# Kernel optimization log

Measured on AMD Instinct MI355X. Metric: run time of the kernel, lower is better.

Reference implementation:

```python
import jax, jax.numpy as jnp
import numpy as np

EMBED_DIM = 768
NUM_HEADS = 12
HEAD_DIM = EMBED_DIM // NUM_HEADS
SCALING = HEAD_DIM ** (-0.5)


def setup_inputs() -> dict:
    key = jax.random.key(0)
    ks = jax.random.split(key, 10)
    R, C, B, E = 128, 256, 1, EMBED_DIM
    x = jax.random.normal(ks[0], (R, C, B, E), dtype=jnp.float32)
    pad_mask = jax.random.randint(ks[1], (B, C), 0, 2).astype(bool)
    s = 1.0 / np.sqrt(E)
    wq = jax.random.normal(ks[2], (E, E), dtype=jnp.float32) * s
    bq = jnp.zeros((E,), dtype=jnp.float32)
    wk = jax.random.normal(ks[3], (E, E), dtype=jnp.float32) * s
    bk = jnp.zeros((E,), dtype=jnp.float32)
    wv = jax.random.normal(ks[4], (E, E), dtype=jnp.float32) * s
    bv = jnp.zeros((E,), dtype=jnp.float32)
    wo = jax.random.normal(ks[5], (E, E), dtype=jnp.float32) * s
    bo = jnp.zeros((E,), dtype=jnp.float32)
    return {"x": x, "self_attn_padding_mask": pad_mask,
            "wq": wq, "bq": bq, "wk": wk, "bk": bk,
            "wv": wv, "bv": bv, "wo": wo, "bo": bo}


def reference(x, self_attn_padding_mask, wq, bq, wk, bk, wv, bv, wo, bo):
    # x: [num_rows R, num_cols C, batch B, embed E]
    R, C, B, E = x.shape
    H, D = NUM_HEADS, HEAD_DIM
    q = (x @ wq.T + bq).reshape(R, C, B, H, D) * SCALING
    k = (x @ wk.T + bk).reshape(R, C, B, H, D)
    v = (x @ wv.T + bv).reshape(R, C, B, H, D)
    # attention over rows, independent per column c and batch n
    attn_weights = jnp.einsum('icnhd,jcnhd->hcnij', q, k)  # [H,C,B,R,R]
    if self_attn_padding_mask is not None:
        # mask: [B,C] -> mask all keys j for padded columns (same for all j)
        m = self_attn_padding_mask.T[None, :, :, None, None]  # [1,C,B,1,1]
        attn_weights = jnp.where(m, jnp.float32(-10000.0), attn_weights)
    attn_probs = jax.nn.softmax(attn_weights, axis=-1)
    context = jnp.einsum('hcnij,jcnhd->icnhd', attn_probs, v)
    context = context.reshape(R, C, B, E)
    output = context @ wo.T + bo
    return output, attn_probs
```

## Files before the change

### kernel.cpp

```cpp
#include <hip/hip_runtime.h>


typedef __attribute__((ext_vector_type(8))) __bf16 bf16x8;
typedef __attribute__((ext_vector_type(4))) float f32x4;
typedef unsigned short u16;
typedef unsigned int u32;

constexpr size_t TE = (size_t)32768 * 768;
constexpr int VSTRIDE = 256 * 1536;

__device__ __forceinline__ u16 f2b(float f) {
    u32 u = __builtin_bit_cast(u32, f);
    u += 0x7FFFu + ((u >> 16) & 1u);
    return (u16)(u >> 16);
}
__device__ __forceinline__ void split2(float f, u16& h, u16& l) {
    u32 u = __builtin_bit_cast(u32, f);
    h = (u16)(u >> 16);
    float rest = f - __builtin_bit_cast(float, u & 0xFFFF0000u);
    l = (u16)(__builtin_bit_cast(u32, rest) >> 16);
}

union B8 { bf16x8 v; u16 s[8]; uint4 q; };

__global__ __launch_bounds__(256) void convert_w3(
    const float* __restrict__ Wq, const float* __restrict__ Wk,
    const float* __restrict__ Wv, u16* __restrict__ slots)
{
    const int m = blockIdx.y;
    const float* src = (m == 0) ? Wq : ((m == 1) ? Wk : Wv);
    const int idx = blockIdx.x * 256 + threadIdx.x;
    const int r = idx / 96, k0 = (idx % 96) * 8;
    float4 f0 = *(const float4*)(src + (size_t)r * 768 + k0);
    float4 f1 = *(const float4*)(src + (size_t)r * 768 + k0 + 4);
    B8 h, l;
    split2(f0.x, h.s[0], l.s[0]); split2(f0.y, h.s[1], l.s[1]);
    split2(f0.z, h.s[2], l.s[2]); split2(f0.w, h.s[3], l.s[3]);
    split2(f1.x, h.s[4], l.s[4]); split2(f1.y, h.s[5], l.s[5]);
    split2(f1.z, h.s[6], l.s[6]); split2(f1.w, h.s[7], l.s[7]);
    *(uint4*)&slots[(size_t)1536 * (m * 1536 + r) + k0] = h.q;
    *(uint4*)&slots[(size_t)1536 * (m * 1536 + 768 + r) + k0] = l.q;
}

template <int MODE>
__global__ __launch_bounds__(256) void gemm_proj(
    const float* __restrict__ A, const u16* __restrict__ wsl, int wbase,
    const float* __restrict__ bias, u16* __restrict__ dst, float scale)
{
    const int wg = ((blockIdx.x & 7) * 192) + (blockIdx.x >> 3);
    const int tm = wg / 6, tn = wg - tm * 6;
    const int tid = threadIdx.x;
    const int lane = tid & 63, w = tid >> 6;
    const int l16 = lane & 15, quad = lane >> 4;
    const int wr = w >> 1, wc = w & 1;

    __shared__ u16 Ah[2][128][4][8], Al[2][128][4][8];

    f32x4 acc[4][4];
#pragma unroll
    for (int a = 0; a < 4; ++a)
#pragma unroll
        for (int b = 0; b < 4; ++b) acc[a][b] = (f32x4){0.f, 0.f, 0.f, 0.f};

    const int row0 = tid >> 3, kq = tid & 7;
    const int c8 = kq >> 1, o4 = (kq & 1) * 4;
    const float* ap = A + ((size_t)tm * 128 + row0) * 768 + kq * 4;

    float4 pf[4];
#define LOADA(k0) do {                                                        \
    _Pragma("unroll")                                                         \
    for (int it = 0; it < 4; ++it)                                            \
        pf[it] = *(const float4*)(ap + (k0) + (size_t)it * 32 * 768);         \
} while (0)

#define STAGE(buf) do {                                                       \
    _Pragma("unroll")                                                         \
    for (int it = 0; it < 4; ++it) {                                          \
        int row = row0 + 32 * it;                                             \
        int sw = c8 ^ (((row >> 1) ^ (row >> 3)) & 3);                        \
        u16 h0,h1,h2,h3,l0,l1,l2,l3;                                          \
        split2(pf[it].x,h0,l0); split2(pf[it].y,h1,l1);                       \
        split2(pf[it].z,h2,l2); split2(pf[it].w,h3,l3);                       \
        *(uint2*)&Ah[buf][row][sw][o4] =                                      \
            make_uint2((u32)h0|((u32)h1<<16),(u32)h2|((u32)h3<<16));          \
        *(uint2*)&Al[buf][row][sw][o4] =                                      \
            make_uint2((u32)l0|((u32)l1<<16),(u32)l2|((u32)l3<<16));          \
    }                                                                         \
} while (0)

    LOADA(0);
    STAGE(0);
    __syncthreads();

    for (int kc = 0; kc < 24; ++kc) {
        const int buf = kc & 1;
        const int k0 = kc * 32;

        bf16x8 bh[4], bl[4];
#pragma unroll
        for (int b = 0; b < 4; ++b) {
            int n = tn * 128 + 64 * wc + 16 * b + l16;
            bh[b] = *(const bf16x8*)&wsl[(size_t)1536 * (wbase + n) + k0 + quad * 8];
            bl[b] = *(const bf16x8*)&wsl[(size_t)1536 * (wbase + 768 + n) + k0 + quad * 8];
        }
        if (kc < 23) LOADA(k0 + 32);

        bf16x8 ah[4], al[4];
#pragma unroll
        for (int a = 0; a < 4; ++a) {
            int row = 64 * wr + 16 * a + l16;
            int sw = quad ^ (((row >> 1) ^ (row >> 3)) & 3);
            ah[a] = *(const bf16x8*)&Ah[buf][row][sw][0];
            al[a] = *(const bf16x8*)&Al[buf][row][sw][0];
        }
#pragma unroll
        for (int a = 0; a < 4; ++a)
#pragma unroll
            for (int b = 0; b < 4; ++b) {
                acc[a][b] = __builtin_amdgcn_mfma_f32_16x16x32_bf16(ah[a], bh[b], acc[a][b], 0, 0, 0);
                acc[a][b] = __builtin_amdgcn_mfma_f32_16x16x32_bf16(ah[a], bl[b], acc[a][b], 0, 0, 0);
                acc[a][b] = __builtin_amdgcn_mfma_f32_16x16x32_bf16(al[a], bh[b], acc[a][b], 0, 0, 0);
            }
        if (kc < 23) STAGE(buf ^ 1);
        __syncthreads();
    }
#undef LOADA
#undef STAGE

#pragma unroll
    for (int b = 0; b < 4; ++b) {
        int n = tn * 128 + 64 * wc + 16 * b + l16;
        float bs = bias[n];
#pragma unroll
        for (int a = 0; a < 4; ++a) {
#pragma unroll
            for (int r = 0; r < 4; ++r) {
                int row = 64 * wr + 16 * a + quad * 4 + r;
                int t = tm * 128 + row;
                float val = (acc[a][b][r] + bs) * scale;
                if (MODE == 2) {
                    dst[(size_t)t * 1536 + 768 + n] = f2b(val);
                } else {
                    int i = t >> 8, cc = t & 255;
                    int hh = n >> 6, d = n & 63;
                    u16* win = dst + (((size_t)hh * 256 + cc) << 15);
                    int base = (MODE == 0 ? 0 : 16384);
                    u16 vh, vl; split2(val, vh, vl);
                    win[base + i * 64 + d] = vh;
                    win[base + 8192 + i * 64 + d] = vl;
                }
            }
        }
    }
}

__global__ __launch_bounds__(256) void attn_kernel(
    u16* __restrict__ winU,
    u16* __restrict__ slots,
    const int* __restrict__ maskg)
{
    const int blk = blockIdx.x;
    const int c = blk & 255, h = blk >> 8;
    const int tid = threadIdx.x;
    const int lane = tid & 63, w = tid >> 6;
    const int l16 = lane & 15, quad = lane >> 4;

    __shared__ u16 kbuf[2][8][128][8];
    __shared__ u16 vsT[16][64][8];
    u16 (*ps)[128][8] = (u16(*)[128][8])&kbuf[0][0][0][0];

    u16* win = winU + (((size_t)h * 256 + c) << 15);
    float* winF = (float*)win;

#pragma unroll
    for (int it = 0; it < 4; ++it) {
        int v = tid + 256 * it;
        int j = v >> 3, d0 = (v & 7) * 8;
        *(uint4*)&kbuf[0][d0 >> 3][j][0] = *(const uint4*)(win + 16384 + j * 64 + d0);
        *(uint4*)&kbuf[1][d0 >> 3][j][0] = *(const uint4*)(win + 24576 + j * 64 + d0);
    }
    const u16* vb = slots + (size_t)c * 1536 + 768 + h * 64;
#pragma unroll
    for (int it = 0; it < 4; ++it) {
        int v = tid + 256 * it;
        int j = v >> 3, d0 = (v & 7) * 8;
        B8 t; t.q = *(const uint4*)(vb + (size_t)j * VSTRIDE + d0);
#pragma unroll
        for (int e = 0; e < 8; ++e) vsT[j >> 3][d0 + e][j & 7] = t.s[e];
    }
    __syncthreads();

    f32x4 s[2][8];
#pragma unroll
    for (int a = 0; a < 2; ++a)
#pragma unroll
        for (int jb = 0; jb < 8; ++jb) s[a][jb] = (f32x4){0.f, 0.f, 0.f, 0.f};

#pragma unroll
    for (int kc = 0; kc < 2; ++kc) {
        bf16x8 qh[2], ql[2];
#pragma unroll
        for (int a = 0; a < 2; ++a) {
            int i = 32 * w + 16 * a + l16;
            qh[a] = *(const bf16x8*)(win + i * 64 + kc * 32 + quad * 8);
            ql[a] = *(const bf16x8*)(win + 8192 + i * 64 + kc * 32 + quad * 8);
        }
#pragma unroll
        for (int jb = 0; jb < 8; ++jb) {
            bf16x8 kh = *(const bf16x8*)&kbuf[0][kc * 4 + quad][16 * jb + l16][0];
            bf16x8 kl = *(const bf16x8*)&kbuf[1][kc * 4 + quad][16 * jb + l16][0];
#pragma unroll
            for (int a = 0; a < 2; ++a) {
                s[a][jb] = __builtin_amdgcn_mfma_f32_16x16x32_bf16(qh[a], kh, s[a][jb], 0, 0, 0);
                s[a][jb] = __builtin_amdgcn_mfma_f32_16x16x32_bf16(qh[a], kl, s[a][jb], 0, 0, 0);
                s[a][jb] = __builtin_amdgcn_mfma_f32_16x16x32_bf16(ql[a], kh, s[a][jb], 0, 0, 0);
            }
        }
    }

    if (maskg[c] != 0) {
#pragma unroll
        for (int a = 0; a < 2; ++a)
#pragma unroll
            for (int jb = 0; jb < 8; ++jb) s[a][jb] = (f32x4){0.f, 0.f, 0.f, 0.f};
    }

#pragma unroll
    for (int a = 0; a < 2; ++a) {
#pragma unroll
        for (int r = 0; r < 4; ++r) {
            float m = s[a][0][r];
#pragma unroll
            for (int jb = 1; jb < 8; ++jb) m = fmaxf(m, s[a][jb][r]);
#pragma unroll
            for (int off = 1; off < 16; off <<= 1) m = fmaxf(m, __shfl_xor(m, off, 64));
            float sum = 0.f;
#pragma unroll
            for (int jb = 0; jb < 8; ++jb) {
                float e = expf(s[a][jb][r] - m);
                s[a][jb][r] = e;
                sum += e;
            }
#pragma unroll
            for (int off = 1; off < 16; off <<= 1) sum += __shfl_xor(sum, off, 64);
            float inv = 1.f / sum;
#pragma unroll
            for (int jb = 0; jb < 8; ++jb) s[a][jb][r] *= inv;
        }
    }

    __syncthreads();

#pragma unroll
    for (int a = 0; a < 2; ++a)
#pragma unroll
        for (int jb = 0; jb < 8; ++jb)
#pragma unroll
            for (int r = 0; r < 4; ++r) {
                int i = 32 * w + 16 * a + quad * 4 + r;
                int j = 16 * jb + l16;
                float pv = s[a][jb][r];
                winF[i * 128 + j] = pv;
                ps[j >> 3][i][j & 7] = f2b(pv);
            }
    __syncthreads();

    f32x4 o[2][4];
#pragma unroll
    for (int a = 0; a < 2; ++a)
#pragma unroll
        for (int b = 0; b < 4; ++b) o[a][b] = (f32x4){0.f, 0.f, 0.f, 0.f};

#pragma unroll
    for (int kc = 0; kc < 4; ++kc) {
        bf16x8 ap[2];
#pragma unroll
        for (int a = 0; a < 2; ++a)
            ap[a] = *(const bf16x8*)&ps[kc * 4 + quad][32 * w + 16 * a + l16][0];
#pragma unroll
        for (int b = 0; b < 4; ++b) {
            bf16x8 bv = *(const bf16x8*)&vsT[kc * 4 + quad][16 * b + l16][0];
#pragma unroll
            for (int a = 0; a < 2; ++a)
                o[a][b] = __builtin_amdgcn_mfma_f32_16x16x32_bf16(ap[a], bv, o[a][b], 0, 0, 0);
        }
    }

#pragma unroll
    for (int a = 0; a < 2; ++a)
#pragma unroll
        for (int b = 0; b < 4; ++b)
#pragma unroll
            for (int r = 0; r < 4; ++r) {
                int i = 32 * w + 16 * a + quad * 4 + r;
                int d = 16 * b + l16;
                slots[(size_t)(i * 256 + c) * 1536 + h * 64 + d] = f2b(o[a][b][r]);
            }
}

__global__ __launch_bounds__(256) void gemm_out(
    const u16* __restrict__ slots, const float* __restrict__ W,
    const float* __restrict__ bias, float* __restrict__ out0, int nb)
{
    const int t0 = blockIdx.x * 64;
    const int tid = threadIdx.x;
    const int lane = tid & 63, w = tid >> 6;
    const int l16 = lane & 15, quad = lane >> 4;

    __shared__ u16 cs[2][4][64][8];

    f32x4 acc[4][6];
#pragma unroll
    for (int a = 0; a < 4; ++a)
#pragma unroll
        for (int jt = 0; jt < 6; ++jt) acc[a][jt] = (f32x4){0.f, 0.f, 0.f, 0.f};

    const int srow = tid >> 2, sk8 = tid & 3;
    const u16* sp = slots + (size_t)(t0 + srow) * 1536 + sk8 * 8;

    *(uint4*)&cs[0][sk8][srow][0] = *(const uint4*)(sp);
    for (int kc = 0; kc < 24; ++kc) {
        const int buf = kc & 1;
        __syncthreads();
        if (kc + 1 < 24)
            *(uint4*)&cs[buf ^ 1][sk8][srow][0] = *(const uint4*)(sp + (kc + 1) * 32);

        bf16x8 af[4];
#pragma unroll
        for (int a = 0; a < 4; ++a)
            af[a] = *(const bf16x8*)&cs[buf][quad][16 * a + l16][0];

#pragma unroll
        for (int jt = 0; jt < 6; ++jt) {
            int n = nb + 96 * w + 16 * jt + l16;
            const float* wp = W + (size_t)n * 768 + kc * 32 + quad * 8;
            float4 f0 = *(const float4*)(wp);
            float4 f1 = *(const float4*)(wp + 4);
            B8 wh, wl;
            split2(f0.x, wh.s[0], wl.s[0]); split2(f0.y, wh.s[1], wl.s[1]);
            split2(f0.z, wh.s[2], wl.s[2]); split2(f0.w, wh.s[3], wl.s[3]);
            split2(f1.x, wh.s[4], wl.s[4]); split2(f1.y, wh.s[5], wl.s[5]);
            split2(f1.z, wh.s[6], wl.s[6]); split2(f1.w, wh.s[7], wl.s[7]);
#pragma unroll
            for (int a = 0; a < 4; ++a) {
                acc[a][jt] = __builtin_amdgcn_mfma_f32_16x16x32_bf16(af[a], wh.v, acc[a][jt], 0, 0, 0);
                acc[a][jt] = __builtin_amdgcn_mfma_f32_16x16x32_bf16(af[a], wl.v, acc[a][jt], 0, 0, 0);
            }
        }
    }

#pragma unroll
    for (int jt = 0; jt < 6; ++jt) {
        int n = nb + 96 * w + 16 * jt + l16;
        float bs = bias[n];
#pragma unroll
        for (int a = 0; a < 4; ++a) {
#pragma unroll
            for (int r = 0; r < 4; ++r) {
                int row = 16 * a + quad * 4 + r;
                out0[(size_t)(t0 + row) * 768 + n] = acc[a][jt][r] + bs;
            }
        }
    }
}

extern "C" void kernel_launch(void* const* d_in, const int* in_sizes, int n_in,
                              void* d_out, int out_size, void* d_ws, size_t ws_size,
                              hipStream_t stream) {
    const float* x    = (const float*)d_in[0];
    const int*   mask = (const int*)d_in[1];
    const float* wq = (const float*)d_in[2];
    const float* bq = (const float*)d_in[3];
    const float* wk = (const float*)d_in[4];
    const float* bk = (const float*)d_in[5];
    const float* wv = (const float*)d_in[6];
    const float* bv = (const float*)d_in[7];
    const float* wo = (const float*)d_in[8];
    const float* bo = (const float*)d_in[9];

    float* out0  = (float*)d_out;
    u16*   slots = (u16*)d_out;
    u16*   winU  = (u16*)(out0 + TE);

    dim3 blk(256);
    convert_w3<<<dim3(288, 3), blk, 0, stream>>>(wq, wk, wv, slots);
    gemm_proj<0><<<dim3(1536), blk, 0, stream>>>(x, slots, 0,    bq, winU,  0.125f);
    gemm_proj<1><<<dim3(1536), blk, 0, stream>>>(x, slots, 1536, bk, winU,  1.0f);
    gemm_proj<2><<<dim3(1536), blk, 0, stream>>>(x, slots, 3072, bv, slots, 1.0f);
    attn_kernel<<<dim3(12 * 256), blk, 0, stream>>>(winU, slots, mask);
    gemm_out<<<dim3(512), blk, 0, stream>>>(slots, wo, bo, out0, 384);
    gemm_out<<<dim3(512), blk, 0, stream>>>(slots, wo, bo, out0, 0);
}
```

Baseline: 1.338 ms.

## Fuse Q, K, V projection GEMMs into one kernel sharing A tiles

Merges the three separate projection GEMM launches into a single kernel with 512 threads. Each block loads and splits its x tile into hi/lo bf16 once and applies it against all three weight matrices, keeping 3x4x2 accumulators per wave. This removes two of the three reads and hi/lo conversions of the large fp32 input. In exchange the per-thread register footprint rises, which may reduce occupancy.

After: 1.346 ms. No clear change (+0.6%).

```diff
diff --git a/kernel.cpp b/kernel.cpp
--- a/kernel.cpp
+++ b/kernel.cpp
@@ -42,41 +42,44 @@
     *(uint4*)&slots[(size_t)1536 * (m * 1536 + 768 + r) + k0] = l.q;
 }
 
-template <int MODE>
-__global__ __launch_bounds__(256) void gemm_proj(
-    const float* __restrict__ A, const u16* __restrict__ wsl, int wbase,
-    const float* __restrict__ bias, u16* __restrict__ dst, float scale)
+__global__ __launch_bounds__(512) void gemm_qkv(
+    const float* __restrict__ A, const u16* __restrict__ wsl,
+    const float* __restrict__ bq, const float* __restrict__ bk,
+    const float* __restrict__ bv,
+    u16* __restrict__ winU, u16* __restrict__ slots)
 {
     const int wg = ((blockIdx.x & 7) * 192) + (blockIdx.x >> 3);
     const int tm = wg / 6, tn = wg - tm * 6;
     const int tid = threadIdx.x;
     const int lane = tid & 63, w = tid >> 6;
     const int l16 = lane & 15, quad = lane >> 4;
-    const int wr = w >> 1, wc = w & 1;
+    const int wr = w >> 2, wc = w & 3;
 
     __shared__ u16 Ah[2][128][4][8], Al[2][128][4][8];
 
-    f32x4 acc[4][4];
-#pragma unroll
-    for (int a = 0; a < 4; ++a)
-#pragma unroll
-        for (int b = 0; b < 4; ++b) acc[a][b] = (f32x4){0.f, 0.f, 0.f, 0.f};
+    f32x4 acc[3][4][2];
+#pragma unroll
+    for (int m = 0; m < 3; ++m)
+#pragma unroll
+        for (int a = 0; a < 4; ++a)
+#pragma unroll
+            for (int b = 0; b < 2; ++b) acc[m][a][b] = (f32x4){0.f, 0.f, 0.f, 0.f};
 
     const int row0 = tid >> 3, kq = tid & 7;
     const int c8 = kq >> 1, o4 = (kq & 1) * 4;
     const float* ap = A + ((size_t)tm * 128 + row0) * 768 + kq * 4;
 
-    float4 pf[4];
+    float4 pf[2];
 #define LOADA(k0) do {                                                        \
     _Pragma("unroll")                                                         \
-    for (int it = 0; it < 4; ++it)                                            \
-        pf[it] = *(const float4*)(ap + (k0) + (size_t)it * 32 * 768);         \
+    for (int it = 0; it < 2; ++it)                                            \
+        pf[it] = *(const float4*)(ap + (k0) + (size_t)it * 64 * 768);         \
 } while (0)
 
 #define STAGE(buf) do {                                                       \
     _Pragma("unroll")                                                         \
-    for (int it = 0; it < 4; ++it) {                                          \
-        int row = row0 + 32 * it;                                             \
+    for (int it = 0; it < 2; ++it) {                                          \
+        int row = row0 + 64 * it;                                             \
         int sw = c8 ^ (((row >> 1) ^ (row >> 3)) & 3);                        \
         u16 h0,h1,h2,h3,l0,l1,l2,l3;                                          \
         split2(pf[it].x,h0,l0); split2(pf[it].y,h1,l1);                       \
@@ -96,13 +99,15 @@
         const int buf = kc & 1;
         const int k0 = kc * 32;
 
-        bf16x8 bh[4], bl[4];
-#pragma unroll
-        for (int b = 0; b < 4; ++b) {
-            int n = tn * 128 + 64 * wc + 16 * b + l16;
-            bh[b] = *(const bf16x8*)&wsl[(size_t)1536 * (wbase + n) + k0 + quad * 8];
-            bl[b] = *(const bf16x8*)&wsl[(size_t)1536 * (wbase + 768 + n) + k0 + quad * 8];
-        }
+        bf16x8 bh[3][2], bl[3][2];
+#pragma unroll
+        for (int m = 0; m < 3; ++m)
+#pragma unroll
+            for (int b = 0; b < 2; ++b) {
+                int n = tn * 128 + 32 * wc + 16 * b + l16;
+                bh[m][b] = *(const bf16x8*)&wsl[(size_t)1536 * (m * 1536 + n) + k0 + quad * 8];
+                bl[m][b] = *(const bf16x8*)&wsl[(size_t)1536 * (m * 1536 + 768 + n) + k0 + quad * 8];
+            }
         if (kc < 23) LOADA(k0 + 32);
 
         bf16x8 ah[4], al[4];
@@ -114,40 +119,47 @@
             al[a] = *(const bf16x8*)&Al[buf][row][sw][0];
         }
 #pragma unroll
-        for (int a = 0; a < 4; ++a)
-#pragma unroll
-            for (int b = 0; b < 4; ++b) {
-                acc[a][b] = __builtin_amdgcn_mfma_f32_16x16x32_bf16(ah[a], bh[b], acc[a][b], 0, 0, 0);
-                acc[a][b] = __builtin_amdgcn_mfma_f32_16x16x32_bf16(ah[a], bl[b], acc[a][b], 0, 0, 0);
-                acc[a][b] = __builtin_amdgcn_mfma_f32_16x16x32_bf16(al[a], bh[b], acc[a][b], 0, 0, 0);
-            }
+        for (int m = 0; m < 3; ++m)
+#pragma unroll
+            for (int a = 0; a < 4; ++a)
+#pragma unroll
+                for (int b = 0; b < 2; ++b) {
+                    acc[m][a][b] = __builtin_amdgcn_mfma_f32_16x16x32_bf16(ah[a], bh[m][b], acc[m][a][b], 0, 0, 0);
+                    acc[m][a][b] = __builtin_amdgcn_mfma_f32_16x16x32_bf16(ah[a], bl[m][b], acc[m][a][b], 0, 0, 0);
+                    acc[m][a][b] = __builtin_amdgcn_mfma_f32_16x16x32_bf16(al[a], bh[m][b], acc[m][a][b], 0, 0, 0);
+                }
         if (kc < 23) STAGE(buf ^ 1);
         __syncthreads();
     }
 #undef LOADA
 #undef STAGE
 
-#pragma unroll
-    for (int b = 0; b < 4; ++b) {
-        int n = tn * 128 + 64 * wc + 16 * b + l16;
-        float bs = bias[n];
-#pragma unroll
-        for (int a = 0; a < 4; ++a) {
-#pragma unroll
-            for (int r = 0; r < 4; ++r) {
-                int row = 64 * wr + 16 * a + quad * 4 + r;
-                int t = tm * 128 + row;
-                float val = (acc[a][b][r] + bs) * scale;
-                if (MODE == 2) {
-                    dst[(size_t)t * 1536 + 768 + n] = f2b(val);
-                } else {
-                    int i = t >> 8, cc = t & 255;
-                    int hh = n >> 6, d = n & 63;
-                    u16* win = dst + (((size_t)hh * 256 + cc) << 15);
-                    int base = (MODE == 0 ? 0 : 16384);
-                    u16 vh, vl; split2(val, vh, vl);
-                    win[base + i * 64 + d] = vh;
-                    win[base + 8192 + i * 64 + d] = vl;
+    const float* biases[3] = {bq, bk, bv};
+#pragma unroll
+    for (int m = 0; m < 3; ++m) {
+        const float scale = (m == 0) ? 0.125f : 1.0f;
+#pragma unroll
+        for (int b = 0; b < 2; ++b) {
+            int n = tn * 128 + 32 * wc + 16 * b + l16;
+            float bs = biases[m][n];
+#pragma unroll
+            for (int a = 0; a < 4; ++a) {
+#pragma unroll
+                for (int r = 0; r < 4; ++r) {
+                    int row = 64 * wr + 16 * a + quad * 4 + r;
+                    int t = tm * 128 + row;
+                    float val = (acc[m][a][b][r] + bs) * scale;
+                    if (m == 2) {
+                        slots[(size_t)t * 1536 + 768 + n] = f2b(val);
+                    } else {
+                        int i = t >> 8, cc = t & 255;
+                        int hh = n >> 6, d = n & 63;
+                        u16* win = winU + (((size_t)hh * 256 + cc) << 15);
+                        int base = (m == 0 ? 0 : 16384);
+                        u16 vh, vl; split2(val, vh, vl);
+                        win[base + i * 64 + d] = vh;
+                        win[base + 8192 + i * 64 + d] = vl;
+                    }
                 }
             }
         }
@@ -382,12 +394,9 @@
     u16*   slots = (u16*)d_out;
     u16*   winU  = (u16*)(out0 + TE);
 
-    dim3 blk(256);
-    convert_w3<<<dim3(288, 3), blk, 0, stream>>>(wq, wk, wv, slots);
-    gemm_proj<0><<<dim3(1536), blk, 0, stream>>>(x, slots, 0,    bq, winU,  0.125f);
-    gemm_proj<1><<<dim3(1536), blk, 0, stream>>>(x, slots, 1536, bk, winU,  1.0f);
-    gemm_proj<2><<<dim3(1536), blk, 0, stream>>>(x, slots, 3072, bv, slots, 1.0f);
-    attn_kernel<<<dim3(12 * 256), blk, 0, stream>>>(winU, slots, mask);
-    gemm_out<<<dim3(512), blk, 0, stream>>>(slots, wo, bo, out0, 384);
-    gemm_out<<<dim3(512), blk, 0, stream>>>(slots, wo, bo, out0, 0);
-}
+    convert_w3<<<dim3(288, 3), dim3(256), 0, stream>>>(wq, wk, wv, slots);
+    gemm_qkv<<<dim3(1536), dim3(512), 0, stream>>>(x, slots, bq, bk, bv, winU, slots);
+    attn_kernel<<<dim3(12 * 256), dim3(256), 0, stream>>>(winU, slots, mask);
+    gemm_out<<<dim3(512), dim3(256), 0, stream>>>(slots, wo, bo, out0, 384);
+    gemm_out<<<dim3(512), dim3(256), 0, stream>>>(slots, wo, bo, out0, 0);
+}
```
